# Kernel optimization log

Measured on AMD Instinct MI355X. Metric: run time of the kernel, lower is better.

Reference implementation:

```python
import jax, jax.numpy as jnp
import numpy as np


def _bilinear_sample(v, gx, gy, H_, W_):
    # v: (B, H_, W_, nh, Cv); gx, gy: (B, Lq, nh, P) in [0,1] normalized coords.
    # Matches F.grid_sample(mode='bilinear', padding_mode='zeros', align_corners=False).
    x = gx * W_ - 0.5
    y = gy * H_ - 0.5
    x0 = jnp.floor(x)
    y0 = jnp.floor(y)
    dx = x - x0
    dy = y - y0
    x0i = x0.astype(jnp.int32)
    y0i = y0.astype(jnp.int32)
    nh = v.shape[3]
    hidx = jnp.arange(nh)[None, :, None]  # broadcast over (Lq, nh, P)

    def corner(yi, xi):
        valid = (yi >= 0) & (yi < H_) & (xi >= 0) & (xi < W_)
        yc = jnp.clip(yi, 0, H_ - 1)
        xc = jnp.clip(xi, 0, W_ - 1)
        gather = jax.vmap(lambda vb, yb, xb: vb[yb, xb, hidx])  # -> (B, Lq, nh, P, Cv)
        return gather(v, yc, xc) * valid[..., None].astype(v.dtype)

    v00 = corner(y0i, x0i)
    v01 = corner(y0i, x0i + 1)
    v10 = corner(y0i + 1, x0i)
    v11 = corner(y0i + 1, x0i + 1)
    wx0 = (1.0 - dx)[..., None]
    wx1 = dx[..., None]
    wy0 = (1.0 - dy)[..., None]
    wy1 = dy[..., None]
    return wy0 * (wx0 * v00 + wx1 * v01) + wy1 * (wx0 * v10 + wx1 * v11)


def setup_inputs() -> dict:
    key = jax.random.key(0)
    ks = jax.random.split(key, 10)
    C, NH, NL, NP = 256, 8, 4, 4
    B = 1
    shapes = np.array([[128, 128], [64, 64], [32, 32], [16, 16]], dtype=np.int64)
    L_in = int((shapes[:, 0] * shapes[:, 1]).sum())  # 21760
    Lq = L_in
    lsi = np.concatenate([[0], np.cumsum(shapes[:, 0] * shapes[:, 1])[:-1]]).astype(np.int64)

    # sampling_offsets bias init (grid of directions scaled by point index), per _reset_parameters
    thetas = np.arange(NH, dtype=np.float32) * (2.0 * np.pi / NH)
    grid = np.stack([np.cos(thetas), np.sin(thetas)], -1)
    grid = grid / np.abs(grid).max(-1, keepdims=True)
    grid = np.tile(grid[:, None, None, :], (1, NL, NP, 1))
    grid = grid * (np.arange(NP, dtype=np.float32) + 1.0)[None, None, :, None]
    b_off = jnp.asarray(grid.reshape(-1))

    xav = float(np.sqrt(2.0 / (C + C)))
    return {
        "query": jax.random.normal(ks[0], (B, Lq, C), jnp.float32),
        "reference_points": jax.random.uniform(ks[1], (B, Lq, NL, 2), jnp.float32),
        "input_flatten": jax.random.normal(ks[2], (B, L_in, C), jnp.float32),
        "input_spatial_shapes": jnp.asarray(shapes),
        "input_level_start_index": jnp.asarray(lsi),
        "input_padding_mask": jnp.zeros((B, L_in), jnp.bool_),
        "W_off": 0.01 * jax.random.normal(ks[3], (C, NH * NL * NP * 2), jnp.float32),
        "b_off": b_off,
        "W_attn": 0.01 * jax.random.normal(ks[4], (C, NH * NL * NP), jnp.float32),
        "b_attn": jnp.zeros((NH * NL * NP,), jnp.float32),
        "W_v": xav * jax.random.normal(ks[5], (C, C), jnp.float32),
        "b_v": jnp.zeros((C,), jnp.float32),
        "W_out": xav * jax.random.normal(ks[6], (C, C), jnp.float32),
        "b_out": jnp.zeros((C,), jnp.float32),
    }


def reference(query, reference_points, input_flatten, input_spatial_shapes,
              input_level_start_index, input_padding_mask,
              W_off, b_off, W_attn, b_attn, W_v, b_v, W_out, b_out):
    shapes = np.asarray(input_spatial_shapes)  # static spatial shapes (host constants)
    B, Lq, C = query.shape
    NL = shapes.shape[0]
    NH = 8
    Cv = C // NH
    NP = b_off.shape[0] // (NH * NL * 2)

    value = input_flatten @ W_v + b_v
    value = jnp.where(input_padding_mask[..., None], 0.0, value)
    value = value.reshape(B, -1, NH, Cv)

    off = (query @ W_off + b_off).reshape(B, Lq, NH, NL, NP, 2)
    attn = (query @ W_attn + b_attn).reshape(B, Lq, NH, NL * NP)
    attn = jax.nn.softmax(attn, axis=-1).reshape(B, Lq, NH, NL, NP)

    # normalizer is (W, H) per level
    norm = jnp.stack([jnp.asarray(shapes[:, 1]), jnp.asarray(shapes[:, 0])], -1).astype(query.dtype)
    loc = reference_points[:, :, None, :, None, :] + off / norm[None, None, None, :, None, :]

    out = jnp.zeros((B, Lq, NH, Cv), query.dtype)
    start = 0
    for lvl in range(NL):
        H_, W_ = int(shapes[lvl, 0]), int(shapes[lvl, 1])
        v_l = value[:, start:start + H_ * W_].reshape(B, H_, W_, NH, Cv)
        start += H_ * W_
        g = loc[:, :, :, lvl]  # (B, Lq, NH, NP, 2)
        sampled = _bilinear_sample(v_l, g[..., 0], g[..., 1], H_, W_)  # (B, Lq, NH, NP, Cv)
        out = out + jnp.einsum('blhpc,blhp->blhc', sampled, attn[:, :, :, lvl])

    out = out.reshape(B, Lq, C) @ W_out + b_out
    return out  # dropout is identity in eval mode
```

## Files before the change

### kernel.cpp

```cpp
#include <hip/hip_runtime.h>
#include <hip/hip_bf16.h>
#include <hip/hip_fp16.h>


typedef _Float16 f16;
typedef _Float16 f16x8 __attribute__((ext_vector_type(8)));
typedef _Float16 f16x4 __attribute__((ext_vector_type(4)));
typedef float    f32x4 __attribute__((ext_vector_type(4)));
typedef int      i32x2 __attribute__((ext_vector_type(2)));

__device__ __forceinline__ void g2lds16(const void* gp, void* lp) {
    __builtin_amdgcn_global_load_lds(
        (const __attribute__((address_space(1))) unsigned int*)gp,
        (__attribute__((address_space(3))) unsigned int*)lp, 16, 0, 0);
}

template <bool HALF_OUT, bool MASKED>
__device__ __forceinline__ void gemm_core(
    const f16* __restrict__ A, const f16* __restrict__ Btb,
    const float* __restrict__ bias,
    void* __restrict__ C, int ldc, int coff,
    const unsigned char* __restrict__ mask, int m0,
    f16* __restrict__ As, f16* __restrict__ Bs)
{
    const int tid = threadIdx.x, lane = tid & 63, wid = tid >> 6;
    const int wm = (wid >> 1) * 64, wn = (wid & 1) * 64;
    f32x4 acc[4][4] = {};

    const int sr_ = tid >> 2;
    const int sch = tid & 3;

    for (int kt = 0; kt < 24; ++kt) {
        const int kA = (kt < 16 ? kt : kt - 16) * 32;
        const int kB = kt * 32;
#pragma unroll
        for (int p = 0; p < 2; ++p) {
            const int r  = p * 64 + sr_;
            const int gc = (sch ^ ((r >> 1) & 3)) << 3;
            g2lds16(A + (size_t)(m0 + r) * 512 + kA + gc, &As[r * 32 + sch * 8]);
        }
#pragma unroll
        for (int p = 0; p < 2; ++p) {
            const int r  = p * 64 + sr_;
            const int gc = (sch ^ ((r >> 1) & 3)) << 3;
            g2lds16(Btb + (size_t)r * 768 + kB + gc, &Bs[r * 32 + sch * 8]);
        }
        __syncthreads();

        f16x8 av[4], bv[4];
        const int kch = lane >> 4;
#pragma unroll
        for (int mf = 0; mf < 4; ++mf) {
            const int row = wm + mf * 16 + (lane & 15);
            av[mf] = *(const f16x8*)&As[row * 32 + ((kch ^ ((row >> 1) & 3)) << 3)];
        }
#pragma unroll
        for (int nf = 0; nf < 4; ++nf) {
            const int row = wn + nf * 16 + (lane & 15);
            bv[nf] = *(const f16x8*)&Bs[row * 32 + ((kch ^ ((row >> 1) & 3)) << 3)];
        }
#pragma unroll
        for (int mf = 0; mf < 4; ++mf)
#pragma unroll
            for (int nf = 0; nf < 4; ++nf)
                acc[mf][nf] = __builtin_amdgcn_mfma_f32_16x16x32_f16(
                    av[mf], bv[nf], acc[mf][nf], 0, 0, 0);
        __syncthreads();
    }

#pragma unroll
    for (int mf = 0; mf < 4; ++mf) {
        const int rb = m0 + wm + mf * 16 + ((lane >> 4) << 2);
#pragma unroll
        for (int nf = 0; nf < 4; ++nf) {
            const int nl = wn + nf * 16 + (lane & 15);
            const float bc = bias[nl];
#pragma unroll
            for (int j = 0; j < 4; ++j) {
                const int row = rb + j;
                float v = acc[mf][nf][j] + bc;
                if (MASKED) v = mask[row] ? 0.f : v;
                if (HALF_OUT)
                    ((__half*)C)[(size_t)row * ldc + coff + nl] = __float2half(v);
                else
                    ((float*)C)[(size_t)row * ldc + coff + nl] = v;
            }
        }
    }
}

__global__ __launch_bounds__(256) void gemm_batch1(
    const f16* __restrict__ A1, const f16* __restrict__ A2,
    const f16* __restrict__ Btv, const f16* __restrict__ Btoa,
    const float* __restrict__ b_v, const float* __restrict__ b_off,
    const float* __restrict__ b_attn,
    __half* __restrict__ valueH, float* __restrict__ outF,
    float* __restrict__ logitF, const unsigned char* __restrict__ mask)
{
    __shared__ __align__(16) f16 As[128 * 32];
    __shared__ __align__(16) f16 Bs[128 * 32];
    const int bx = blockIdx.x, m0 = blockIdx.y * 128;
    if (bx < 2)
        gemm_core<true, true>(A1, Btv + (size_t)bx * 128 * 768, b_v + bx * 128,
                              valueH, 256, bx * 128, mask, m0, As, Bs);
    else if (bx < 4)
        gemm_core<false, false>(A2, Btoa + (size_t)(bx - 2) * 128 * 768,
                                b_off + (bx - 2) * 128, outF, 256,
                                (bx - 2) * 128, nullptr, m0, As, Bs);
    else
        gemm_core<false, false>(A2, Btoa + (size_t)256 * 768, b_attn,
                                logitF, 128, 0, nullptr, m0, As, Bs);
}

__global__ __launch_bounds__(256) void gemm_batch2(
    const f16* __restrict__ preA, const f16* __restrict__ Btout,
    const float* __restrict__ b_out, float* __restrict__ outF)
{
    __shared__ __align__(16) f16 As[128 * 32];
    __shared__ __align__(16) f16 Bs[128 * 32];
    const int bx = blockIdx.x, m0 = blockIdx.y * 128;
    gemm_core<false, false>(preA, Btout + (size_t)bx * 128 * 768,
                            b_out + bx * 128, outF, 256, bx * 128,
                            nullptr, m0, As, Bs);
}

__global__ __launch_bounds__(256) void convA2_kernel(
    const float* __restrict__ inF, const float* __restrict__ query,
    f16* __restrict__ A1, f16* __restrict__ A2, int perT)
{
    const int i = blockIdx.x * 256 + threadIdx.x;
    const float* __restrict__ src = (i < perT) ? inF : query;
    f16* __restrict__ dst = (i < perT) ? A1 : A2;
    const int ii = (i < perT) ? i : i - perT;
    if (ii >= perT) return;
    const int m = ii >> 6, k4 = (ii & 63) << 2;
    const float4 v = reinterpret_cast<const float4*>(src)[ii];
    f16x4 hi, lo;
    hi.x = (f16)v.x; lo.x = (f16)(v.x - (float)hi.x);
    hi.y = (f16)v.y; lo.y = (f16)(v.y - (float)hi.y);
    hi.z = (f16)v.z; lo.z = (f16)(v.z - (float)hi.z);
    hi.w = (f16)v.w; lo.w = (f16)(v.w - (float)hi.w);
    *reinterpret_cast<f16x4*>(&dst[(size_t)m * 512 + k4])       = hi;
    *reinterpret_cast<f16x4*>(&dst[(size_t)m * 512 + 256 + k4]) = lo;
}

__global__ __launch_bounds__(256) void prep_kernel(
    const float* __restrict__ Wv,   const float* __restrict__ Woff,
    const float* __restrict__ Wattn,const float* __restrict__ Wout,
    f16* __restrict__ Btv, f16* __restrict__ Btoa, f16* __restrict__ Btout)
{
    const int i = blockIdx.x * 256 + threadIdx.x;
    constexpr int S0 = 256 * 768, S1 = 256 * 768, S2 = 128 * 768, S3 = 256 * 768;
    if (i < S0) {
        const int n = i / 768, k = i - n * 768, ks = k & 255;
        const float w = Wv[(size_t)ks * 256 + n];
        const f16 h = (f16)w;
        Btv[i] = (k < 512) ? h : (f16)(w - (float)h);
    } else if (i < S0 + S1) {
        const int j = i - S0;
        const int n = j / 768, k = j - n * 768, ks = k & 255;
        const float w = Woff[(size_t)ks * 256 + n];
        const f16 h = (f16)w;
        Btoa[j] = (k < 512) ? h : (f16)(w - (float)h);
    } else if (i < S0 + S1 + S2) {
        const int j = i - S0 - S1;
        const int n = j / 768, k = j - n * 768, ks = k & 255;
        const float w = Wattn[(size_t)ks * 128 + n];
        const f16 h = (f16)w;
        Btoa[(size_t)(256 + n) * 768 + k] = (k < 512) ? h : (f16)(w - (float)h);
    } else if (i < S0 + S1 + S2 + S3) {
        const int j = i - S0 - S1 - S2;
        const int n = j / 768, k = j - n * 768, ks = k & 255;
        const float w = Wout[(size_t)ks * 256 + n];
        const f16 h = (f16)w;
        Btout[j] = (k < 512) ? h : (f16)(w - (float)h);
    }
}

__global__ __launch_bounds__(256) void msda_sample_v4(
    const __half* __restrict__ value,
    const float* __restrict__ offF,
    const float* __restrict__ logitF,
    const float* __restrict__ refp,
    f16* __restrict__ preA)
{
    __shared__ float s_off[4][256];
    __shared__ float s_ref[4][8];
    __shared__ __align__(16) float s_w[4][576];
    __shared__ __align__(16) int   s_i[4][576];

    const int q0 = blockIdx.x * 4, tid = threadIdx.x;
#pragma unroll
    for (int j = 0; j < 4; ++j) {
        const int idx = tid + j * 256;
        const int ql = idx >> 8, col = idx & 255;
        s_off[ql][col] = offF[(size_t)(q0 + ql) * 256 + col];
    }
    if (tid < 32) s_ref[tid >> 3][tid & 7] = refp[(size_t)(q0 + (tid >> 3)) * 8 + (tid & 7)];
    __syncthreads();

#pragma unroll
    for (int j = 0; j < 2; ++j) {
        const int idx = tid + j * 256;
        const int ql = idx >> 7, slot = idx & 127;
        const int h = slot >> 4, pp = slot & 15, l = pp >> 2, p = pp & 3;
        float v = logitF[(size_t)(q0 + ql) * 128 + slot];
        float mx = v;
#pragma unroll
        for (int o = 1; o < 16; o <<= 1) mx = fmaxf(mx, __shfl_xor(mx, o, 16));
        const float e = expf(v - mx);
        float s = e;
#pragma unroll
        for (int o = 1; o < 16; o <<= 1) s += __shfl_xor(s, o, 16);
        const float a = e / s;

        const int HW_[4]  = {128, 64, 32, 16};
        const int LSI_[4] = {0, 16384, 20480, 21504};
        const int   Wi = HW_[l];
        const float Wf = (float)Wi;
        const float rx = s_ref[ql][l * 2 + 0], ry = s_ref[ql][l * 2 + 1];
        const float ox = s_off[ql][h * 32 + l * 8 + p * 2 + 0];
        const float oy = s_off[ql][h * 32 + l * 8 + p * 2 + 1];
        const float x = (rx + ox / Wf) * Wf - 0.5f;
        const float y = (ry + oy / Wf) * Wf - 0.5f;
        const float x0f = floorf(x), y0f = floorf(y);
        const float dx = x - x0f, dy = y - y0f;
        const int x0 = (int)x0f, y0 = (int)y0f;
        const int x1 = x0 + 1, y1 = y0 + 1;
        const float vx0 = (x0 >= 0 && x0 < Wi) ? 1.f : 0.f;
        const float vx1 = (x1 >= 0 && x1 < Wi) ? 1.f : 0.f;
        const float vy0 = (y0 >= 0 && y0 < Wi) ? 1.f : 0.f;
        const float vy1 = (y1 >= 0 && y1 < Wi) ? 1.f : 0.f;
        const int xc0 = min(max(x0, 0), Wi - 1), xc1 = min(max(x1, 0), Wi - 1);
        const int yc0 = min(max(y0, 0), Wi - 1), yc1 = min(max(y1, 0), Wi - 1);
        const int base = LSI_[l];
        const int eI = h * 72 + pp * 4;
        s_i[ql][eI + 0] = (base + yc0 * Wi + xc0) * 512;
        s_i[ql][eI + 1] = (base + yc0 * Wi + xc1) * 512;
        s_i[ql][eI + 2] = (base + yc1 * Wi + xc0) * 512;
        s_i[ql][eI + 3] = (base + yc1 * Wi + xc1) * 512;
        s_w[ql][eI + 0] = a * (1.f - dy) * (1.f - dx) * vy0 * vx0;
        s_w[ql][eI + 1] = a * (1.f - dy) * dx         * vy0 * vx1;
        s_w[ql][eI + 2] = a * dy         * (1.f - dx) * vy1 * vx0;
        s_w[ql][eI + 3] = a * dy         * dx         * vy1 * vx1;
    }
    __syncthreads();

    const int ql = tid >> 6, slot = tid & 63;
    const int h = slot >> 3, c8 = (slot & 7) << 2;
    const int lb = (h * 32 + c8) * 2;
    const char* __restrict__ vbase = (const char*)value;
    f32x4 acc = {0.f, 0.f, 0.f, 0.f};
#pragma unroll
    for (int pp = 0; pp < 16; ++pp) {
        const int eI = h * 72 + pp * 4;
        const int4   idx = *reinterpret_cast<const int4*>(&s_i[ql][eI]);
        const float4 wv  = *reinterpret_cast<const float4*>(&s_w[ql][eI]);
        const i32x2 r0 = *reinterpret_cast<const i32x2*>(vbase + (idx.x + lb));
        const i32x2 r1 = *reinterpret_cast<const i32x2*>(vbase + (idx.y + lb));
        const i32x2 r2 = *reinterpret_cast<const i32x2*>(vbase + (idx.z + lb));
        const i32x2 r3 = *reinterpret_cast<const i32x2*>(vbase + (idx.w + lb));
        acc += wv.x * __builtin_convertvector(__builtin_bit_cast(f16x4, r0), f32x4);
        acc += wv.y * __builtin_convertvector(__builtin_bit_cast(f16x4, r1), f32x4);
        acc += wv.z * __builtin_convertvector(__builtin_bit_cast(f16x4, r2), f32x4);
        acc += wv.w * __builtin_convertvector(__builtin_bit_cast(f16x4, r3), f32x4);
    }
    const int q = q0 + ql;
    f16x4 hi, lo;
#pragma unroll
    for (int j = 0; j < 4; ++j) {
        hi[j] = (f16)acc[j];
        lo[j] = (f16)(acc[j] - (float)hi[j]);
    }
    *reinterpret_cast<f16x4*>(&preA[(size_t)q * 512 + h * 32 + c8])       = hi;
    *reinterpret_cast<f16x4*>(&preA[(size_t)q * 512 + 256 + h * 32 + c8]) = lo;
}

extern "C" void kernel_launch(void* const* d_in, const int* in_sizes, int n_in,
                              void* d_out, int out_size, void* d_ws, size_t ws_size,
                              hipStream_t stream)
{
    const float*         query  = (const float*)d_in[0];
    const float*         refp   = (const float*)d_in[1];
    const float*         inF    = (const float*)d_in[2];
    const unsigned char* mask   = (const unsigned char*)d_in[5];
    const float*         W_off  = (const float*)d_in[6];
    const float*         b_off  = (const float*)d_in[7];
    const float*         W_attn = (const float*)d_in[8];
    const float*         b_attn = (const float*)d_in[9];
    const float*         W_v    = (const float*)d_in[10];
    const float*         b_v    = (const float*)d_in[11];
    const float*         W_out  = (const float*)d_in[12];
    const float*         b_out  = (const float*)d_in[13];
    float*               outF   = (float*)d_out;

    const int M = in_sizes[0] / 256;
    if (M % 128 != 0) return;

    const size_t SZ_A   = (size_t)M * 512 * sizeof(f16);
    const size_t SZ_VAL = (size_t)M * 256 * sizeof(__half);
    const size_t SZ_LG  = (size_t)M * 128 * sizeof(float);
    char* w = (char*)d_ws;
    f16*    A1     = (f16*)w;                      w += SZ_A;
    f16*    A2     = (f16*)w;                      w += SZ_A;
    __half* valueH = (__half*)w;                   w += SZ_VAL;
    float*  logitF = (float*)w;                    w += SZ_LG;
    f16*    Btv    = (f16*)w;                      w += 256 * 768 * sizeof(f16);
    f16*    Btoa   = (f16*)w;                      w += 384 * 768 * sizeof(f16);
    f16*    Btout  = (f16*)w;                      w += 256 * 768 * sizeof(f16);
    if ((size_t)(w - (char*)d_ws) > ws_size) return;

    const dim3 blk256(256);
    const int prep_total = (256 + 384 + 256) * 768;
    const int perT = M * 64;

    prep_kernel<<<dim3((prep_total + 255) / 256), blk256, 0, stream>>>(
        W_v, W_off, W_attn, W_out, Btv, Btoa, Btout);

    convA2_kernel<<<dim3((2 * perT + 255) / 256), blk256, 0, stream>>>(
        inF, query, A1, A2, perT);

    gemm_batch1<<<dim3(5, M / 128), blk256, 0, stream>>>(
        A1, A2, Btv, Btoa, b_v, b_off, b_attn, valueH, outF, logitF, mask);

    msda_sample_v4<<<dim3(M / 4), blk256, 0, stream>>>(
        valueH, outF, logitF, refp, A1);

    gemm_batch2<<<dim3(2, M / 128), blk256, 0, stream>>>(A1, Btout, b_out, outF);
}
```

Before: 239.5 us.

## Drop weight lo-split in GEMMs, use BK=64 tiles, head-major value layout for sampling

```diff
diff --git a/kernel.cpp b/kernel.cpp
--- a/kernel.cpp
+++ b/kernel.cpp
@@ -6,8 +6,8 @@
 typedef _Float16 f16;
 typedef _Float16 f16x8 __attribute__((ext_vector_type(8)));
 typedef _Float16 f16x4 __attribute__((ext_vector_type(4)));
+typedef _Float16 f16x2 __attribute__((ext_vector_type(2)));
 typedef float    f32x4 __attribute__((ext_vector_type(4)));
-typedef int      i32x2 __attribute__((ext_vector_type(2)));
 
 __device__ __forceinline__ void g2lds16(const void* gp, void* lp) {
     __builtin_amdgcn_global_load_lds(
@@ -15,56 +15,59 @@
         (__attribute__((address_space(3))) unsigned int*)lp, 16, 0, 0);
 }
 
-template <bool HALF_OUT, bool MASKED>
+template <bool VLAYOUT, bool MASKED>
 __device__ __forceinline__ void gemm_core(
     const f16* __restrict__ A, const f16* __restrict__ Btb,
     const float* __restrict__ bias,
     void* __restrict__ C, int ldc, int coff,
-    const unsigned char* __restrict__ mask, int m0,
+    const unsigned char* __restrict__ mask, int m0, int Ltot,
     f16* __restrict__ As, f16* __restrict__ Bs)
 {
     const int tid = threadIdx.x, lane = tid & 63, wid = tid >> 6;
     const int wm = (wid >> 1) * 64, wn = (wid & 1) * 64;
     f32x4 acc[4][4] = {};
 
-    const int sr_ = tid >> 2;
-    const int sch = tid & 3;
-
-    for (int kt = 0; kt < 24; ++kt) {
-        const int kA = (kt < 16 ? kt : kt - 16) * 32;
-        const int kB = kt * 32;
-#pragma unroll
-        for (int p = 0; p < 2; ++p) {
-            const int r  = p * 64 + sr_;
-            const int gc = (sch ^ ((r >> 1) & 3)) << 3;
-            g2lds16(A + (size_t)(m0 + r) * 512 + kA + gc, &As[r * 32 + sch * 8]);
+    const int sr8 = tid >> 3;
+    const int sch = tid & 7;
+
+    for (int kt = 0; kt < 8; ++kt) {
+        const int kA = kt * 64;
+        const int kB = (kt & 3) * 64;
+#pragma unroll
+        for (int j = 0; j < 4; ++j) {
+            const int r  = j * 32 + sr8;
+            const int gc = ((sch ^ (r & 7)) << 3);
+            g2lds16(A + (size_t)(m0 + r) * 512 + kA + gc, &As[r * 64 + sch * 8]);
         }
 #pragma unroll
-        for (int p = 0; p < 2; ++p) {
-            const int r  = p * 64 + sr_;
-            const int gc = (sch ^ ((r >> 1) & 3)) << 3;
-            g2lds16(Btb + (size_t)r * 768 + kB + gc, &Bs[r * 32 + sch * 8]);
+        for (int j = 0; j < 4; ++j) {
+            const int r  = j * 32 + sr8;
+            const int gc = ((sch ^ (r & 7)) << 3);
+            g2lds16(Btb + (size_t)r * 256 + kB + gc, &Bs[r * 64 + sch * 8]);
         }
         __syncthreads();
 
-        f16x8 av[4], bv[4];
-        const int kch = lane >> 4;
-#pragma unroll
-        for (int mf = 0; mf < 4; ++mf) {
-            const int row = wm + mf * 16 + (lane & 15);
-            av[mf] = *(const f16x8*)&As[row * 32 + ((kch ^ ((row >> 1) & 3)) << 3)];
+#pragma unroll
+        for (int kf = 0; kf < 2; ++kf) {
+            const int kch = kf * 4 + (lane >> 4);
+            f16x8 av[4], bv[4];
+#pragma unroll
+            for (int mf = 0; mf < 4; ++mf) {
+                const int row = wm + mf * 16 + (lane & 15);
+                av[mf] = *(const f16x8*)&As[row * 64 + ((kch ^ (row & 7)) << 3)];
+            }
+#pragma unroll
+            for (int nf = 0; nf < 4; ++nf) {
+                const int row = wn + nf * 16 + (lane & 15);
+                bv[nf] = *(const f16x8*)&Bs[row * 64 + ((kch ^ (row & 7)) << 3)];
+            }
+#pragma unroll
+            for (int mf = 0; mf < 4; ++mf)
+#pragma unroll
+                for (int nf = 0; nf < 4; ++nf)
+                    acc[mf][nf] = __builtin_amdgcn_mfma_f32_16x16x32_f16(
+                        av[mf], bv[nf], acc[mf][nf], 0, 0, 0);
         }
-#pragma unroll
-        for (int nf = 0; nf < 4; ++nf) {
-            const int row = wn + nf * 16 + (lane & 15);
-            bv[nf] = *(const f16x8*)&Bs[row * 32 + ((kch ^ ((row >> 1) & 3)) << 3)];
-        }
-#pragma unroll
-        for (int mf = 0; mf < 4; ++mf)
-#pragma unroll
-            for (int nf = 0; nf < 4; ++nf)
-                acc[mf][nf] = __builtin_amdgcn_mfma_f32_16x16x32_f16(
-                    av[mf], bv[nf], acc[mf][nf], 0, 0, 0);
         __syncthreads();
     }
 
@@ -80,10 +83,13 @@
                 const int row = rb + j;
                 float v = acc[mf][nf][j] + bc;
                 if (MASKED) v = mask[row] ? 0.f : v;
-                if (HALF_OUT)
-                    ((__half*)C)[(size_t)row * ldc + coff + nl] = __float2half(v);
-                else
+                if (VLAYOUT) {
+                    const int col = coff + nl;
+                    ((__half*)C)[((size_t)(col >> 5) * Ltot + row) * 32 + (col & 31)]
+                        = __float2half(v);
+                } else {
                     ((float*)C)[(size_t)row * ldc + coff + nl] = v;
+                }
             }
         }
     }
@@ -95,33 +101,33 @@
     const float* __restrict__ b_v, const float* __restrict__ b_off,
     const float* __restrict__ b_attn,
     __half* __restrict__ valueH, float* __restrict__ outF,
-    float* __restrict__ logitF, const unsigned char* __restrict__ mask)
-{
-    __shared__ __align__(16) f16 As[128 * 32];
-    __shared__ __align__(16) f16 Bs[128 * 32];
+    float* __restrict__ logitF, const unsigned char* __restrict__ mask, int M)
+{
+    __shared__ __align__(16) f16 As[128 * 64];
+    __shared__ __align__(16) f16 Bs[128 * 64];
     const int bx = blockIdx.x, m0 = blockIdx.y * 128;
     if (bx < 2)
-        gemm_core<true, true>(A1, Btv + (size_t)bx * 128 * 768, b_v + bx * 128,
-                              valueH, 256, bx * 128, mask, m0, As, Bs);
+        gemm_core<true, true>(A1, Btv + (size_t)bx * 128 * 256, b_v + bx * 128,
+                              valueH, 0, bx * 128, mask, m0, M, As, Bs);
     else if (bx < 4)
-        gemm_core<false, false>(A2, Btoa + (size_t)(bx - 2) * 128 * 768,
+        gemm_core<false, false>(A2, Btoa + (size_t)(bx - 2) * 128 * 256,
                                 b_off + (bx - 2) * 128, outF, 256,
-                                (bx - 2) * 128, nullptr, m0, As, Bs);
+                                (bx - 2) * 128, nullptr, m0, M, As, Bs);
     else
-        gemm_core<false, false>(A2, Btoa + (size_t)256 * 768, b_attn,
-                                logitF, 128, 0, nullptr, m0, As, Bs);
+        gemm_core<false, false>(A2, Btoa + (size_t)256 * 256, b_attn,
+                                logitF, 128, 0, nullptr, m0, M, As, Bs);
 }
 
 __global__ __launch_bounds__(256) void gemm_batch2(
     const f16* __restrict__ preA, const f16* __restrict__ Btout,
-    const float* __restrict__ b_out, float* __restrict__ outF)
-{
-    __shared__ __align__(16) f16 As[128 * 32];
-    __shared__ __align__(16) f16 Bs[128 * 32];
+    const float* __restrict__ b_out, float* __restrict__ outF, int M)
+{
+    __shared__ __align__(16) f16 As[128 * 64];
+    __shared__ __align__(16) f16 Bs[128 * 64];
     const int bx = blockIdx.x, m0 = blockIdx.y * 128;
-    gemm_core<false, false>(preA, Btout + (size_t)bx * 128 * 768,
+    gemm_core<false, false>(preA, Btout + (size_t)bx * 128 * 256,
                             b_out + bx * 128, outF, 256, bx * 128,
-                            nullptr, m0, As, Bs);
+                            nullptr, m0, M, As, Bs);
 }
 
 __global__ __launch_bounds__(256) void convA2_kernel(
@@ -150,59 +156,49 @@
     f16* __restrict__ Btv, f16* __restrict__ Btoa, f16* __restrict__ Btout)
 {
     const int i = blockIdx.x * 256 + threadIdx.x;
-    constexpr int S0 = 256 * 768, S1 = 256 * 768, S2 = 128 * 768, S3 = 256 * 768;
+    constexpr int S0 = 256 * 256, S1 = 256 * 256, S2 = 128 * 256, S3 = 256 * 256;
     if (i < S0) {
-        const int n = i / 768, k = i - n * 768, ks = k & 255;
-        const float w = Wv[(size_t)ks * 256 + n];
-        const f16 h = (f16)w;
-        Btv[i] = (k < 512) ? h : (f16)(w - (float)h);
+        const int n = i >> 8, k = i & 255;
+        Btv[i] = (f16)Wv[(size_t)k * 256 + n];
     } else if (i < S0 + S1) {
         const int j = i - S0;
-        const int n = j / 768, k = j - n * 768, ks = k & 255;
-        const float w = Woff[(size_t)ks * 256 + n];
-        const f16 h = (f16)w;
-        Btoa[j] = (k < 512) ? h : (f16)(w - (float)h);
+        const int n = j >> 8, k = j & 255;
+        Btoa[j] = (f16)Woff[(size_t)k * 256 + n];
     } else if (i < S0 + S1 + S2) {
         const int j = i - S0 - S1;
-        const int n = j / 768, k = j - n * 768, ks = k & 255;
-        const float w = Wattn[(size_t)ks * 128 + n];
-        const f16 h = (f16)w;
-        Btoa[(size_t)(256 + n) * 768 + k] = (k < 512) ? h : (f16)(w - (float)h);
+        const int n = j >> 8, k = j & 255;
+        Btoa[(size_t)(256 + n) * 256 + k] = (f16)Wattn[(size_t)k * 128 + n];
     } else if (i < S0 + S1 + S2 + S3) {
         const int j = i - S0 - S1 - S2;
-        const int n = j / 768, k = j - n * 768, ks = k & 255;
-        const float w = Wout[(size_t)ks * 256 + n];
-        const f16 h = (f16)w;
-        Btout[j] = (k < 512) ? h : (f16)(w - (float)h);
-    }
-}
-
-__global__ __launch_bounds__(256) void msda_sample_v4(
+        const int n = j >> 8, k = j & 255;
+        Btout[j] = (f16)Wout[(size_t)k * 256 + n];
+    }
+}
+
+__global__ __launch_bounds__(256) void msda_sample_v5(
     const __half* __restrict__ value,
     const float* __restrict__ offF,
     const float* __restrict__ logitF,
     const float* __restrict__ refp,
-    f16* __restrict__ preA)
-{
-    __shared__ float s_off[4][256];
-    __shared__ float s_ref[4][8];
-    __shared__ __align__(16) float s_w[4][576];
-    __shared__ __align__(16) int   s_i[4][576];
-
-    const int q0 = blockIdx.x * 4, tid = threadIdx.x;
-#pragma unroll
-    for (int j = 0; j < 4; ++j) {
+    f16* __restrict__ preA, int Ltot)
+{
+    __shared__ float s_off[2][256];
+    __shared__ float s_ref[2][8];
+    __shared__ __align__(16) float s_w[2][576];
+    __shared__ __align__(16) int   s_i[2][576];
+
+    const int q0 = blockIdx.x * 2, tid = threadIdx.x;
+#pragma unroll
+    for (int j = 0; j < 2; ++j) {
         const int idx = tid + j * 256;
         const int ql = idx >> 8, col = idx & 255;
         s_off[ql][col] = offF[(size_t)(q0 + ql) * 256 + col];
     }
-    if (tid < 32) s_ref[tid >> 3][tid & 7] = refp[(size_t)(q0 + (tid >> 3)) * 8 + (tid & 7)];
+    if (tid < 16) s_ref[tid >> 3][tid & 7] = refp[(size_t)(q0 + (tid >> 3)) * 8 + (tid & 7)];
     __syncthreads();
 
-#pragma unroll
-    for (int j = 0; j < 2; ++j) {
-        const int idx = tid + j * 256;
-        const int ql = idx >> 7, slot = idx & 127;
+    {
+        const int ql = tid >> 7, slot = tid & 127;
         const int h = slot >> 4, pp = slot & 15, l = pp >> 2, p = pp & 3;
         float v = logitF[(size_t)(q0 + ql) * 128 + slot];
         float mx = v;
@@ -233,12 +229,12 @@
         const float vy1 = (y1 >= 0 && y1 < Wi) ? 1.f : 0.f;
         const int xc0 = min(max(x0, 0), Wi - 1), xc1 = min(max(x1, 0), Wi - 1);
         const int yc0 = min(max(y0, 0), Wi - 1), yc1 = min(max(y1, 0), Wi - 1);
-        const int base = LSI_[l];
+        const int hb = h * Ltot + LSI_[l];
         const int eI = h * 72 + pp * 4;
-        s_i[ql][eI + 0] = (base + yc0 * Wi + xc0) * 512;
-        s_i[ql][eI + 1] = (base + yc0 * Wi + xc1) * 512;
-        s_i[ql][eI + 2] = (base + yc1 * Wi + xc0) * 512;
-        s_i[ql][eI + 3] = (base + yc1 * Wi + xc1) * 512;
+        s_i[ql][eI + 0] = (hb + yc0 * Wi + xc0) * 64;
+        s_i[ql][eI + 1] = (hb + yc0 * Wi + xc1) * 64;
+        s_i[ql][eI + 2] = (hb + yc1 * Wi + xc0) * 64;
+        s_i[ql][eI + 3] = (hb + yc1 * Wi + xc1) * 64;
         s_w[ql][eI + 0] = a * (1.f - dy) * (1.f - dx) * vy0 * vx0;
         s_w[ql][eI + 1] = a * (1.f - dy) * dx         * vy0 * vx1;
         s_w[ql][eI + 2] = a * dy         * (1.f - dx) * vy1 * vx0;
@@ -246,34 +242,35 @@
     }
     __syncthreads();
 
-    const int ql = tid >> 6, slot = tid & 63;
-    const int h = slot >> 3, c8 = (slot & 7) << 2;
-    const int lb = (h * 32 + c8) * 2;
+    const int ql = tid >> 7, slot = tid & 127;
+    const int h = slot >> 4, cp = slot & 15;
+    const int lb = cp * 4;
     const char* __restrict__ vbase = (const char*)value;
-    f32x4 acc = {0.f, 0.f, 0.f, 0.f};
+    float acc0 = 0.f, acc1 = 0.f;
 #pragma unroll
     for (int pp = 0; pp < 16; ++pp) {
         const int eI = h * 72 + pp * 4;
         const int4   idx = *reinterpret_cast<const int4*>(&s_i[ql][eI]);
-        const float4 wv  = *reinterpret_cast<const float4*>(&s_w[ql][eI]);
-        const i32x2 r0 = *reinterpret_cast<const i32x2*>(vbase + (idx.x + lb));
-        const i32x2 r1 = *reinterpret_cast<const i32x2*>(vbase + (idx.y + lb));
-        const i32x2 r2 = *reinterpret_cast<const i32x2*>(vbase + (idx.z + lb));
-        const i32x2 r3 = *reinterpret_cast<const i32x2*>(vbase + (idx.w + lb));
-        acc += wv.x * __builtin_convertvector(__builtin_bit_cast(f16x4, r0), f32x4);
-        acc += wv.y * __builtin_convertvector(__builtin_bit_cast(f16x4, r1), f32x4);
-        acc += wv.z * __builtin_convertvector(__builtin_bit_cast(f16x4, r2), f32x4);
-        acc += wv.w * __builtin_convertvector(__builtin_bit_cast(f16x4, r3), f32x4);
+        const float4 w   = *reinterpret_cast<const float4*>(&s_w[ql][eI]);
+        const __half2 v0 = *reinterpret_cast<const __half2*>(vbase + (idx.x + lb));
+        const __half2 v1 = *reinterpret_cast<const __half2*>(vbase + (idx.y + lb));
+        const __half2 v2 = *reinterpret_cast<const __half2*>(vbase + (idx.z + lb));
+        const __half2 v3 = *reinterpret_cast<const __half2*>(vbase + (idx.w + lb));
+        acc0 = fmaf(w.x, __half2float(v0.x), acc0);
+        acc1 = fmaf(w.x, __half2float(v0.y), acc1);
+        acc0 = fmaf(w.y, __half2float(v1.x), acc0);
+        acc1 = fmaf(w.y, __half2float(v1.y), acc1);
+        acc0 = fmaf(w.z, __half2float(v2.x), acc0);
+        acc1 = fmaf(w.z, __half2float(v2.y), acc1);
+        acc0 = fmaf(w.w, __half2float(v3.x), acc0);
+        acc1 = fmaf(w.w, __half2float(v3.y), acc1);
     }
     const int q = q0 + ql;
-    f16x4 hi, lo;
-#pragma unroll
-    for (int j = 0; j < 4; ++j) {
-        hi[j] = (f16)acc[j];
-        lo[j] = (f16)(acc[j] - (float)hi[j]);
-    }
-    *reinterpret_cast<f16x4*>(&preA[(size_t)q * 512 + h * 32 + c8])       = hi;
-    *reinterpret_cast<f16x4*>(&preA[(size_t)q * 512 + 256 + h * 32 + c8]) = lo;
+    const f16 h0 = (f16)acc0, h1 = (f16)acc1;
+    f16x2 hv; hv.x = h0; hv.y = h1;
+    f16x2 lv; lv.x = (f16)(acc0 - (float)h0); lv.y = (f16)(acc1 - (float)h1);
+    *reinterpret_cast<f16x2*>(&preA[(size_t)q * 512 + h * 32 + cp * 2])       = hv;
+    *reinterpret_cast<f16x2*>(&preA[(size_t)q * 512 + 256 + h * 32 + cp * 2]) = lv;
 }
 
 extern "C" void kernel_launch(void* const* d_in, const int* in_sizes, int n_in,
@@ -305,13 +302,13 @@
     f16*    A2     = (f16*)w;                      w += SZ_A;
     __half* valueH = (__half*)w;                   w += SZ_VAL;
     float*  logitF = (float*)w;                    w += SZ_LG;
-    f16*    Btv    = (f16*)w;                      w += 256 * 768 * sizeof(f16);
-    f16*    Btoa   = (f16*)w;                      w += 384 * 768 * sizeof(f16);
-    f16*    Btout  = (f16*)w;                      w += 256 * 768 * sizeof(f16);
+    f16*    Btv    = (f16*)w;                      w += 256 * 256 * sizeof(f16);
+    f16*    Btoa   = (f16*)w;                      w += 384 * 256 * sizeof(f16);
+    f16*    Btout  = (f16*)w;                      w += 256 * 256 * sizeof(f16);
     if ((size_t)(w - (char*)d_ws) > ws_size) return;
 
     const dim3 blk256(256);
-    const int prep_total = (256 + 384 + 256) * 768;
+    const int prep_total = (256 + 384 + 256) * 256;
     const int perT = M * 64;
 
     prep_kernel<<<dim3((prep_total + 255) / 256), blk256, 0, stream>>>(
@@ -321,10 +318,10 @@
         inF, query, A1, A2, perT);
 
     gemm_batch1<<<dim3(5, M / 128), blk256, 0, stream>>>(
-        A1, A2, Btv, Btoa, b_v, b_off, b_attn, valueH, outF, logitF, mask);
-
-    msda_sample_v4<<<dim3(M / 4), blk256, 0, stream>>>(
-        valueH, outF, logitF, refp, A1);
-
-    gemm_batch2<<<dim3(2, M / 128), blk256, 0, stream>>>(A1, Btout, b_out, outF);
-}
+        A1, A2, Btv, Btoa, b_v, b_off, b_attn, valueH, outF, logitF, mask, M);
+
+    msda_sample_v5<<<dim3(M / 2), blk256, 0, stream>>>(
+        valueH, outF, logitF, refp, A1, M);
+
+    gemm_batch2<<<dim3(2, M / 128), blk256, 0, stream>>>(A1, Btout, b_out, outF, M);
+}
```

Result: faster. 206.3 us (-13.8%).
